# Optimization experiments

Measured on AMD Instinct MI355X. Metric: run time of the kernel, lower is better.

The kernel has to match this reference:

```python
import jax, jax.numpy as jnp
import numpy as np

B, P, C, F, E = 8, 65536, 32768, 32, 524288  # batch, n_paths, n_channels, feature, edges


def setup_inputs() -> dict:
    key = jax.random.key(0)
    ks = jax.random.split(key, 8)
    path_features = jax.random.normal(ks[0], (B, P, F), jnp.float32)
    channel_features = jax.random.normal(ks[1], (B, C, F), jnp.float32)
    edge_path = jax.random.randint(ks[2], (E,), 0, P)
    edge_channel = jnp.sort(jax.random.randint(ks[3], (E,), 0, C))
    s = 1.0 / np.sqrt(F)  # PyTorch GRU default init range
    W_ih = jax.random.uniform(ks[4], (3 * F, F), jnp.float32, -s, s)
    W_hh = jax.random.uniform(ks[5], (3 * F, F), jnp.float32, -s, s)
    b_ih = jax.random.uniform(ks[6], (3 * F,), jnp.float32, -s, s)
    b_hh = jax.random.uniform(ks[7], (3 * F,), jnp.float32, -s, s)
    return dict(path_features=path_features, channel_features=channel_features,
                W_ih=W_ih, W_hh=W_hh, b_ih=b_ih, b_hh=b_hh,
                edge_path=edge_path, edge_channel=edge_channel)


def reference(path_features, channel_features, W_ih, W_hh, b_ih, b_hh, edge_path, edge_channel):
    # Ragged per-channel sum of path features (segment-sum over edge list)
    gathered = jnp.swapaxes(path_features[:, edge_path, :], 0, 1)          # [E, B, F]
    agg = jax.ops.segment_sum(gathered, edge_channel, num_segments=C)      # [C, B, F]
    x = jnp.swapaxes(agg, 0, 1)                                            # [B, C, F]
    h = channel_features                                                   # [B, C, F]
    # Single-step GRU (PyTorch gate order: r, z, n)
    gx = x @ W_ih.T + b_ih                                                 # [B, C, 3F]
    gh = h @ W_hh.T + b_hh
    xr, xz, xn = jnp.split(gx, 3, axis=-1)
    hr, hz, hn = jnp.split(gh, 3, axis=-1)
    r = jax.nn.sigmoid(xr + hr)
    z = jax.nn.sigmoid(xz + hz)
    n = jnp.tanh(xn + r * hn)
    return (1.0 - z) * n + z * h                                           # [B, C, F]
```

## Files before the change

### kernel.cpp

```cpp
#include <hip/hip_runtime.h>

#define NB 8
#define NP 65536
#define NC 32768
#define NF 32
#define NE 524288
#define XROW 40

typedef __attribute__((ext_vector_type(4))) float floatx4;
typedef __attribute__((ext_vector_type(8))) short short8;
typedef __attribute__((ext_vector_type(4))) short short4v;

__device__ __forceinline__ short f2b(float f) {
    union { float f; unsigned int u; } v;
    v.f = f;
    unsigned int lsb = (v.u >> 16) & 1u;
    v.u += 0x7fffu + lsb;
    return (short)(v.u >> 16);
}

__device__ __forceinline__ int lower_bound(const int* __restrict__ a, int v) {
    int lo = 0, hi = NE;
    while (lo < hi) {
        int mid = (lo + hi) >> 1;
        if (a[mid] < v) lo = mid + 1; else hi = mid;
    }
    return lo;
}

__device__ __forceinline__ float sigmoidf_(float v) {
    return 1.f / (1.f + __expf(-v));
}
__device__ __forceinline__ float tanhf_(float v) {
    v = fminf(v, 40.f);
    float t = __expf(2.f * v);
    return (t - 1.f) / (t + 1.f);
}

__global__ __launch_bounds__(256) void fused_gru_kernel(
    const float* __restrict__ path,
    const float* __restrict__ hbuf,
    const float* __restrict__ W_ih,
    const float* __restrict__ W_hh,
    const float* __restrict__ b_ih,
    const float* __restrict__ b_hh,
    const int*   __restrict__ edge_path,
    const int*   __restrict__ edge_channel,
    float*       __restrict__ out)
{
    const int t    = threadIdx.x;
    const int w    = t >> 6;
    const int lane = t & 63;
    const int cblk = blockIdx.x * 8;

    __shared__ int bounds[9];
    __shared__ __align__(16) short xs [64 * XROW];
    __shared__ __align__(16) short wsx[96 * XROW];
    __shared__ __align__(16) short wsh[96 * XROW];

    if (t < 9) bounds[t] = lower_bound(edge_channel, cblk + t);

    for (int idx = t; idx < 96 * NF; idx += 256) {
        int r = idx >> 5, c = idx & 31;
        wsx[r * XROW + c] = f2b(W_ih[idx]);
        wsh[r * XROW + c] = f2b(W_hh[idx]);
    }
    __syncthreads();

    const int b  = lane >> 3;
    const int fq = lane & 7;
    const float* prow = path + (size_t)b * (NP * NF) + fq * 4;

    #pragma unroll
    for (int half = 0; half < 2; ++half) {
        const int cl = w * 2 + half;
        const int s = __builtin_amdgcn_readfirstlane(bounds[cl]);
        const int e = __builtin_amdgcn_readfirstlane(bounds[cl + 1]);
        floatx4 acc = {0.f, 0.f, 0.f, 0.f};
        int i = s;
        for (; i + 8 <= e; i += 8) {
            int p0 = edge_path[i + 0], p1 = edge_path[i + 1];
            int p2 = edge_path[i + 2], p3 = edge_path[i + 3];
            int p4 = edge_path[i + 4], p5 = edge_path[i + 5];
            int p6 = edge_path[i + 6], p7 = edge_path[i + 7];
            floatx4 g0 = *(const floatx4*)(prow + (size_t)p0 * NF);
            floatx4 g1 = *(const floatx4*)(prow + (size_t)p1 * NF);
            floatx4 g2 = *(const floatx4*)(prow + (size_t)p2 * NF);
            floatx4 g3 = *(const floatx4*)(prow + (size_t)p3 * NF);
            floatx4 g4 = *(const floatx4*)(prow + (size_t)p4 * NF);
            floatx4 g5 = *(const floatx4*)(prow + (size_t)p5 * NF);
            floatx4 g6 = *(const floatx4*)(prow + (size_t)p6 * NF);
            floatx4 g7 = *(const floatx4*)(prow + (size_t)p7 * NF);
            acc += ((g0 + g1) + (g2 + g3)) + ((g4 + g5) + (g6 + g7));
        }
        for (; i + 2 <= e; i += 2) {
            int p0 = edge_path[i], p1 = edge_path[i + 1];
            acc += *(const floatx4*)(prow + (size_t)p0 * NF)
                 + *(const floatx4*)(prow + (size_t)p1 * NF);
        }
        if (i < e)
            acc += *(const floatx4*)(prow + (size_t)edge_path[i] * NF);

        short4v xb;
        #pragma unroll
        for (int q = 0; q < 4; ++q) xb[q] = f2b(acc[q]);
        *(short4v*)(&xs[(b * 8 + cl) * XROW + fq * 4]) = xb;
    }
    __syncthreads();

    const int quad = lane >> 4;
    const int n16  = lane & 15;
    const int k0   = quad * 8;

    const int rA = w * 16 + n16;
    short8 ax = *(const short8*)(&xs[rA * XROW + k0]);

    const int bA = rA >> 3;
    const int cA = cblk + (rA & 7);
    const float* hrow = hbuf + ((size_t)bA * NC + cA) * NF + k0;
    floatx4 h0 = *(const floatx4*)(hrow);
    floatx4 h1 = *(const floatx4*)(hrow + 4);
    short8 ah;
    #pragma unroll
    for (int q = 0; q < 4; ++q) { ah[q] = f2b(h0[q]); ah[4 + q] = f2b(h1[q]); }

    float bxv[6], bhv[6];
    #pragma unroll
    for (int tt = 0; tt < 6; ++tt) {
        bxv[tt] = b_ih[16 * tt + n16];
        bhv[tt] = b_hh[16 * tt + n16];
    }

    const floatx4 zero = {0.f, 0.f, 0.f, 0.f};
    floatx4 g[4];
    #pragma unroll
    for (int tt = 0; tt < 4; ++tt) {
        short8 bw = *(const short8*)(&wsx[(16 * tt + n16) * XROW + k0]);
        floatx4 a = __builtin_amdgcn_mfma_f32_16x16x32_bf16(ax, bw, zero, 0, 0, 0);
        bw = *(const short8*)(&wsh[(16 * tt + n16) * XROW + k0]);
        g[tt] = __builtin_amdgcn_mfma_f32_16x16x32_bf16(ah, bw, a, 0, 0, 0);
    }
    floatx4 nx[2], nh[2];
    #pragma unroll
    for (int u = 0; u < 2; ++u) {
        const int tt = 4 + u;
        short8 bw = *(const short8*)(&wsx[(16 * tt + n16) * XROW + k0]);
        nx[u] = __builtin_amdgcn_mfma_f32_16x16x32_bf16(ax, bw, zero, 0, 0, 0);
        bw = *(const short8*)(&wsh[(16 * tt + n16) * XROW + k0]);
        nh[u] = __builtin_amdgcn_mfma_f32_16x16x32_bf16(ah, bw, zero, 0, 0, 0);
    }

    #pragma unroll
    for (int i = 0; i < 4; ++i) {
        const int r  = w * 16 + quad * 4 + i;
        const int b2 = r >> 3;
        const size_t m = (size_t)b2 * NC + (cblk + (r & 7));
        float r0 = sigmoidf_(g[0][i] + bxv[0] + bhv[0]);
        float r1 = sigmoidf_(g[1][i] + bxv[1] + bhv[1]);
        float z0 = sigmoidf_(g[2][i] + bxv[2] + bhv[2]);
        float z1 = sigmoidf_(g[3][i] + bxv[3] + bhv[3]);
        float n0 = tanhf_(nx[0][i] + bxv[4] + r0 * (nh[0][i] + bhv[4]));
        float n1 = tanhf_(nx[1][i] + bxv[5] + r1 * (nh[1][i] + bhv[5]));
        float hv0 = hbuf[m * NF + n16];
        float hv1 = hbuf[m * NF + 16 + n16];
        out[m * NF + n16]      = (1.f - z0) * n0 + z0 * hv0;
        out[m * NF + 16 + n16] = (1.f - z1) * n1 + z1 * hv1;
    }
}

extern "C" void kernel_launch(void* const* d_in, const int* in_sizes, int n_in,
                              void* d_out, int out_size, void* d_ws, size_t ws_size,
                              hipStream_t stream) {
    const float* path = (const float*)d_in[0];
    const float* chan = (const float*)d_in[1];
    const float* W_ih = (const float*)d_in[2];
    const float* W_hh = (const float*)d_in[3];
    const float* b_ih = (const float*)d_in[4];
    const float* b_hh = (const float*)d_in[5];
    const int* edge_path    = (const int*)d_in[6];
    const int* edge_channel = (const int*)d_in[7];
    float* out = (float*)d_out;

    fused_gru_kernel<<<dim3(NC / 8), dim3(256), 0, stream>>>(
        path, chan, W_ih, W_hh, b_ih, b_hh, edge_path, edge_channel, out);
}
```

Before: 222.4 us.

## Pre-transpose path features to path-major fp16 layout for contiguous gathers

Adds a pre-pass kernel that rewrites path_features from [B,P,F] fp32 into a path-major [P,B,F] fp16 buffer in the workspace. The gather loop in the fused GRU kernel then reads all 8 batches of one path from a single contiguous 512-byte row, converting fp16 back to fp32 before accumulating. The aim is to halve the gather traffic and improve locality of the random accesses. In exchange it adds a full read of the path tensor plus a write of the fp16 copy on every call, and loses precision in the inputs before summation. The original fp32 path is kept as a fallback when the workspace is too small.

```diff
diff --git a/kernel.cpp b/kernel.cpp
--- a/kernel.cpp
+++ b/kernel.cpp
@@ -1,4 +1,5 @@
 #include <hip/hip_runtime.h>
+#include <hip/hip_fp16.h>
 
 #define NB 8
 #define NP 65536
@@ -11,6 +12,15 @@
 typedef __attribute__((ext_vector_type(8))) short short8;
 typedef __attribute__((ext_vector_type(4))) short short4v;
 
+struct h4 { __half2 lo, hi; };
+
+__device__ __forceinline__ floatx4 h4tof4(h4 v) {
+    float2 a = __half22float2(v.lo);
+    float2 b = __half22float2(v.hi);
+    floatx4 r; r[0] = a.x; r[1] = a.y; r[2] = b.x; r[3] = b.y;
+    return r;
+}
+
 __device__ __forceinline__ short f2b(float f) {
     union { float f; unsigned int u; } v;
     v.f = f;
@@ -37,16 +47,32 @@
     return (t - 1.f) / (t + 1.f);
 }
 
+__global__ __launch_bounds__(256) void transpose_kernel(
+    const float* __restrict__ path, __half* __restrict__ pathT)
+{
+    const int id = blockIdx.x * 256 + threadIdx.x;
+    const int f4 = (id & 7) * 4;
+    const int b  = (id >> 3) & 7;
+    const int p  = id >> 6;
+    floatx4 v = *(const floatx4*)(path + ((size_t)b * NP + p) * NF + f4);
+    h4 o;
+    o.lo = __floats2half2_rn(v[0], v[1]);
+    o.hi = __floats2half2_rn(v[2], v[3]);
+    *(h4*)(pathT + (size_t)p * (NB * NF) + b * NF + f4) = o;
+}
+
+template <int USET>
 __global__ __launch_bounds__(256) void fused_gru_kernel(
-    const float* __restrict__ path,
-    const float* __restrict__ hbuf,
-    const float* __restrict__ W_ih,
-    const float* __restrict__ W_hh,
-    const float* __restrict__ b_ih,
-    const float* __restrict__ b_hh,
-    const int*   __restrict__ edge_path,
-    const int*   __restrict__ edge_channel,
-    float*       __restrict__ out)
+    const float*  __restrict__ path,
+    const __half* __restrict__ pathT,
+    const float*  __restrict__ hbuf,
+    const float*  __restrict__ W_ih,
+    const float*  __restrict__ W_hh,
+    const float*  __restrict__ b_ih,
+    const float*  __restrict__ b_hh,
+    const int*    __restrict__ edge_path,
+    const int*    __restrict__ edge_channel,
+    float*        __restrict__ out)
 {
     const int t    = threadIdx.x;
     const int w    = t >> 6;
@@ -69,7 +95,8 @@
 
     const int b  = lane >> 3;
     const int fq = lane & 7;
-    const float* prow = path + (size_t)b * (NP * NF) + fq * 4;
+    const float*  prow  = path  + (size_t)b * (NP * NF) + fq * 4;
+    const __half* prowT = pathT + b * NF + fq * 4;
 
     #pragma unroll
     for (int half = 0; half < 2; ++half) {
@@ -78,28 +105,55 @@
         const int e = __builtin_amdgcn_readfirstlane(bounds[cl + 1]);
         floatx4 acc = {0.f, 0.f, 0.f, 0.f};
         int i = s;
-        for (; i + 8 <= e; i += 8) {
-            int p0 = edge_path[i + 0], p1 = edge_path[i + 1];
-            int p2 = edge_path[i + 2], p3 = edge_path[i + 3];
-            int p4 = edge_path[i + 4], p5 = edge_path[i + 5];
-            int p6 = edge_path[i + 6], p7 = edge_path[i + 7];
-            floatx4 g0 = *(const floatx4*)(prow + (size_t)p0 * NF);
-            floatx4 g1 = *(const floatx4*)(prow + (size_t)p1 * NF);
-            floatx4 g2 = *(const floatx4*)(prow + (size_t)p2 * NF);
-            floatx4 g3 = *(const floatx4*)(prow + (size_t)p3 * NF);
-            floatx4 g4 = *(const floatx4*)(prow + (size_t)p4 * NF);
-            floatx4 g5 = *(const floatx4*)(prow + (size_t)p5 * NF);
-            floatx4 g6 = *(const floatx4*)(prow + (size_t)p6 * NF);
-            floatx4 g7 = *(const floatx4*)(prow + (size_t)p7 * NF);
-            acc += ((g0 + g1) + (g2 + g3)) + ((g4 + g5) + (g6 + g7));
+        if (USET) {
+            for (; i + 8 <= e; i += 8) {
+                int p0 = edge_path[i + 0], p1 = edge_path[i + 1];
+                int p2 = edge_path[i + 2], p3 = edge_path[i + 3];
+                int p4 = edge_path[i + 4], p5 = edge_path[i + 5];
+                int p6 = edge_path[i + 6], p7 = edge_path[i + 7];
+                h4 g0 = *(const h4*)(prowT + (size_t)p0 * (NB * NF));
+                h4 g1 = *(const h4*)(prowT + (size_t)p1 * (NB * NF));
+                h4 g2 = *(const h4*)(prowT + (size_t)p2 * (NB * NF));
+                h4 g3 = *(const h4*)(prowT + (size_t)p3 * (NB * NF));
+                h4 g4 = *(const h4*)(prowT + (size_t)p4 * (NB * NF));
+                h4 g5 = *(const h4*)(prowT + (size_t)p5 * (NB * NF));
+                h4 g6 = *(const h4*)(prowT + (size_t)p6 * (NB * NF));
+                h4 g7 = *(const h4*)(prowT + (size_t)p7 * (NB * NF));
+                acc += ((h4tof4(g0) + h4tof4(g1)) + (h4tof4(g2) + h4tof4(g3)))
+                     + ((h4tof4(g4) + h4tof4(g5)) + (h4tof4(g6) + h4tof4(g7)));
+            }
+            for (; i + 2 <= e; i += 2) {
+                int p0 = edge_path[i], p1 = edge_path[i + 1];
+                h4 g0 = *(const h4*)(prowT + (size_t)p0 * (NB * NF));
+                h4 g1 = *(const h4*)(prowT + (size_t)p1 * (NB * NF));
+                acc += h4tof4(g0) + h4tof4(g1);
+            }
+            if (i < e)
+                acc += h4tof4(*(const h4*)(prowT + (size_t)edge_path[i] * (NB * NF)));
+        } else {
+            for (; i + 8 <= e; i += 8) {
+                int p0 = edge_path[i + 0], p1 = edge_path[i + 1];
+                int p2 = edge_path[i + 2], p3 = edge_path[i + 3];
+                int p4 = edge_path[i + 4], p5 = edge_path[i + 5];
+                int p6 = edge_path[i + 6], p7 = edge_path[i + 7];
+                floatx4 g0 = *(const floatx4*)(prow + (size_t)p0 * NF);
+                floatx4 g1 = *(const floatx4*)(prow + (size_t)p1 * NF);
+                floatx4 g2 = *(const floatx4*)(prow + (size_t)p2 * NF);
+                floatx4 g3 = *(const floatx4*)(prow + (size_t)p3 * NF);
+                floatx4 g4 = *(const floatx4*)(prow + (size_t)p4 * NF);
+                floatx4 g5 = *(const floatx4*)(prow + (size_t)p5 * NF);
+                floatx4 g6 = *(const floatx4*)(prow + (size_t)p6 * NF);
+                floatx4 g7 = *(const floatx4*)(prow + (size_t)p7 * NF);
+                acc += ((g0 + g1) + (g2 + g3)) + ((g4 + g5) + (g6 + g7));
+            }
+            for (; i + 2 <= e; i += 2) {
+                int p0 = edge_path[i], p1 = edge_path[i + 1];
+                acc += *(const floatx4*)(prow + (size_t)p0 * NF)
+                     + *(const floatx4*)(prow + (size_t)p1 * NF);
+            }
+            if (i < e)
+                acc += *(const floatx4*)(prow + (size_t)edge_path[i] * NF);
         }
-        for (; i + 2 <= e; i += 2) {
-            int p0 = edge_path[i], p1 = edge_path[i + 1];
-            acc += *(const floatx4*)(prow + (size_t)p0 * NF)
-                 + *(const floatx4*)(prow + (size_t)p1 * NF);
-        }
-        if (i < e)
-            acc += *(const floatx4*)(prow + (size_t)edge_path[i] * NF);
 
         short4v xb;
         #pragma unroll
@@ -181,6 +235,16 @@
     const int* edge_channel = (const int*)d_in[7];
     float* out = (float*)d_out;
 
-    fused_gru_kernel<<<dim3(NC / 8), dim3(256), 0, stream>>>(
-        path, chan, W_ih, W_hh, b_ih, b_hh, edge_path, edge_channel, out);
-}
+    const size_t needT = (size_t)NP * NB * NF * sizeof(__half);
+    if (ws_size >= needT) {
+        __half* pathT = (__half*)d_ws;
+        transpose_kernel<<<dim3((NP * NB * NF / 4) / 256), dim3(256), 0, stream>>>(
+            path, pathT);
+        fused_gru_kernel<1><<<dim3(NC / 8), dim3(256), 0, stream>>>(
+            path, pathT, chan, W_ih, W_hh, b_ih, b_hh, edge_path, edge_channel, out);
+    } else {
+        fused_gru_kernel<0><<<dim3(NC / 8), dim3(256), 0, stream>>>(
+            path, (const __half*)nullptr, chan, W_ih, W_hh, b_ih, b_hh,
+            edge_path, edge_channel, out);
+    }
+}
```

After: 222.3 us. No clear change (-0.0%).

## Convert path features to fp16 in a prep pass and regroup gather by batch

Applied to the files above, without the earlier changes.

Adds a prep kernel that converts the whole path tensor to fp16 in workspace and precomputes all channel segment bounds. The main kernel then gathers half-precision rows. Each block handles one batch over 64 channels, with 8 edges gathered in parallel per wave and reduced by shuffles. Output uses nontemporal stores. The point is to halve the bytes moved by the random gather and drop the per-block binary searches, but the conversion pass must read 64MB and write 32MB every call, which may cost more than the gather saves. fp16 also adds precision loss.

```diff
diff --git a/kernel.cpp b/kernel.cpp
--- a/kernel.cpp
+++ b/kernel.cpp
@@ -1,4 +1,5 @@
 #include <hip/hip_runtime.h>
+#include <hip/hip_fp16.h>
 
 #define NB 8
 #define NP 65536
@@ -6,10 +7,22 @@
 #define NF 32
 #define NE 524288
 #define XROW 40
+#define CHB 64
+#define CONV_BLOCKS 8192
 
 typedef __attribute__((ext_vector_type(4))) float floatx4;
 typedef __attribute__((ext_vector_type(8))) short short8;
 typedef __attribute__((ext_vector_type(4))) short short4v;
+
+struct h4 { __half2 lo, hi; };
+struct h8 { __half2 a, b, c, d; };
+
+__device__ __forceinline__ floatx4 h4tof4(h4 v) {
+    float2 a = __half22float2(v.lo);
+    float2 b = __half22float2(v.hi);
+    floatx4 r; r[0] = a.x; r[1] = a.y; r[2] = b.x; r[3] = b.y;
+    return r;
+}
 
 __device__ __forceinline__ short f2b(float f) {
     union { float f; unsigned int u; } v;
@@ -37,16 +50,156 @@
     return (t - 1.f) / (t + 1.f);
 }
 
-__global__ __launch_bounds__(256) void fused_gru_kernel(
-    const float* __restrict__ path,
-    const float* __restrict__ hbuf,
-    const float* __restrict__ W_ih,
-    const float* __restrict__ W_hh,
-    const float* __restrict__ b_ih,
-    const float* __restrict__ b_hh,
-    const int*   __restrict__ edge_path,
-    const int*   __restrict__ edge_channel,
-    float*       __restrict__ out)
+__global__ __launch_bounds__(256) void prep_kernel(
+    const float* __restrict__ path, __half* __restrict__ pathH,
+    const int* __restrict__ edge_channel, int* __restrict__ bounds)
+{
+    if (blockIdx.x < CONV_BLOCKS) {
+        const size_t id = ((size_t)blockIdx.x * 256 + threadIdx.x) * 8;
+        floatx4 v0 = *(const floatx4*)(path + id);
+        floatx4 v1 = *(const floatx4*)(path + id + 4);
+        h8 o;
+        o.a = __floats2half2_rn(v0[0], v0[1]);
+        o.b = __floats2half2_rn(v0[2], v0[3]);
+        o.c = __floats2half2_rn(v1[0], v1[1]);
+        o.d = __floats2half2_rn(v1[2], v1[3]);
+        *(h8*)(pathH + id) = o;
+    } else {
+        const int c = (blockIdx.x - CONV_BLOCKS) * 256 + threadIdx.x;
+        if (c <= NC) bounds[c] = lower_bound(edge_channel, c);
+    }
+}
+
+__global__ __launch_bounds__(256) void fused_gru_new(
+    const __half* __restrict__ pathH,
+    const float*  __restrict__ hbuf,
+    const float*  __restrict__ W_ih,
+    const float*  __restrict__ W_hh,
+    const float*  __restrict__ b_ih,
+    const float*  __restrict__ b_hh,
+    const int*    __restrict__ edge_path,
+    const int*    __restrict__ bounds,
+    float*        __restrict__ out)
+{
+    const int t    = threadIdx.x;
+    const int w    = t >> 6;
+    const int lane = t & 63;
+    const int batch = blockIdx.x & 7;
+    const int c0    = (blockIdx.x >> 3) * CHB;
+
+    __shared__ __align__(16) short xs [64 * XROW];
+    __shared__ __align__(16) short wsx[96 * XROW];
+    __shared__ __align__(16) short wsh[96 * XROW];
+
+    for (int idx = t; idx < 96 * NF; idx += 256) {
+        int r = idx >> 5, c = idx & 31;
+        wsx[r * XROW + c] = f2b(W_ih[idx]);
+        wsh[r * XROW + c] = f2b(W_hh[idx]);
+    }
+
+    const int eslot = lane >> 3;
+    const int fq    = lane & 7;
+    const __half* pbase = pathH + (size_t)batch * (NP * NF) + fq * 4;
+
+    for (int j = 0; j < 16; ++j) {
+        const int r = w * 16 + j;
+        const int c = c0 + r;
+        const int s = __builtin_amdgcn_readfirstlane(bounds[c]);
+        const int e = __builtin_amdgcn_readfirstlane(bounds[c + 1]);
+        floatx4 acc = {0.f, 0.f, 0.f, 0.f};
+        for (int i = s; i < e; i += 8) {
+            const int idx  = i + eslot;
+            const int idxc = idx < e ? idx : e - 1;
+            const int p    = edge_path[idxc];
+            union { h4 g; uint2 u; } gv;
+            gv.g = *(const h4*)(pbase + (size_t)p * NF);
+            if (idx >= e) { gv.u.x = 0u; gv.u.y = 0u; }
+            acc += h4tof4(gv.g);
+        }
+        #pragma unroll
+        for (int m = 8; m <= 32; m <<= 1) {
+            acc[0] += __shfl_xor(acc[0], m);
+            acc[1] += __shfl_xor(acc[1], m);
+            acc[2] += __shfl_xor(acc[2], m);
+            acc[3] += __shfl_xor(acc[3], m);
+        }
+        if (eslot == 0) {
+            short4v xb;
+            #pragma unroll
+            for (int q = 0; q < 4; ++q) xb[q] = f2b(acc[q]);
+            *(short4v*)(&xs[r * XROW + fq * 4]) = xb;
+        }
+    }
+    __syncthreads();
+
+    const int quad = lane >> 4;
+    const int n16  = lane & 15;
+    const int k0   = quad * 8;
+
+    const int rA = w * 16 + n16;
+    short8 ax = *(const short8*)(&xs[rA * XROW + k0]);
+
+    const size_t mrow = (size_t)batch * NC + c0;
+    const float* hrow = hbuf + (mrow + rA) * NF + k0;
+    floatx4 h0 = *(const floatx4*)(hrow);
+    floatx4 h1 = *(const floatx4*)(hrow + 4);
+    short8 ah;
+    #pragma unroll
+    for (int q = 0; q < 4; ++q) { ah[q] = f2b(h0[q]); ah[4 + q] = f2b(h1[q]); }
+
+    float bxv[6], bhv[6];
+    #pragma unroll
+    for (int tt = 0; tt < 6; ++tt) {
+        bxv[tt] = b_ih[16 * tt + n16];
+        bhv[tt] = b_hh[16 * tt + n16];
+    }
+
+    const floatx4 zero = {0.f, 0.f, 0.f, 0.f};
+    floatx4 g[4];
+    #pragma unroll
+    for (int tt = 0; tt < 4; ++tt) {
+        short8 bw = *(const short8*)(&wsx[(16 * tt + n16) * XROW + k0]);
+        floatx4 a = __builtin_amdgcn_mfma_f32_16x16x32_bf16(ax, bw, zero, 0, 0, 0);
+        bw = *(const short8*)(&wsh[(16 * tt + n16) * XROW + k0]);
+        g[tt] = __builtin_amdgcn_mfma_f32_16x16x32_bf16(ah, bw, a, 0, 0, 0);
+    }
+    floatx4 nx[2], nh[2];
+    #pragma unroll
+    for (int u = 0; u < 2; ++u) {
+        const int tt = 4 + u;
+        short8 bw = *(const short8*)(&wsx[(16 * tt + n16) * XROW + k0]);
+        nx[u] = __builtin_amdgcn_mfma_f32_16x16x32_bf16(ax, bw, zero, 0, 0, 0);
+        bw = *(const short8*)(&wsh[(16 * tt + n16) * XROW + k0]);
+        nh[u] = __builtin_amdgcn_mfma_f32_16x16x32_bf16(ah, bw, zero, 0, 0, 0);
+    }
+
+    #pragma unroll
+    for (int i = 0; i < 4; ++i) {
+        const int r2 = w * 16 + quad * 4 + i;
+        const size_t m = mrow + r2;
+        float r0 = sigmoidf_(g[0][i] + bxv[0] + bhv[0]);
+        float r1 = sigmoidf_(g[1][i] + bxv[1] + bhv[1]);
+        float z0 = sigmoidf_(g[2][i] + bxv[2] + bhv[2]);
+        float z1 = sigmoidf_(g[3][i] + bxv[3] + bhv[3]);
+        float n0 = tanhf_(nx[0][i] + bxv[4] + r0 * (nh[0][i] + bhv[4]));
+        float n1 = tanhf_(nx[1][i] + bxv[5] + r1 * (nh[1][i] + bhv[5]));
+        float hv0 = hbuf[m * NF + n16];
+        float hv1 = hbuf[m * NF + 16 + n16];
+        __builtin_nontemporal_store((1.f - z0) * n0 + z0 * hv0, &out[m * NF + n16]);
+        __builtin_nontemporal_store((1.f - z1) * n1 + z1 * hv1, &out[m * NF + 16 + n16]);
+    }
+}
+
+__global__ __launch_bounds__(256) void fused_gru_fb(
+    const float*  __restrict__ path,
+    const float*  __restrict__ hbuf,
+    const float*  __restrict__ W_ih,
+    const float*  __restrict__ W_hh,
+    const float*  __restrict__ b_ih,
+    const float*  __restrict__ b_hh,
+    const int*    __restrict__ edge_path,
+    const int*    __restrict__ edge_channel,
+    float*        __restrict__ out)
 {
     const int t    = threadIdx.x;
     const int w    = t >> 6;
@@ -59,7 +212,6 @@
     __shared__ __align__(16) short wsh[96 * XROW];
 
     if (t < 9) bounds[t] = lower_bound(edge_channel, cblk + t);
-
     for (int idx = t; idx < 96 * NF; idx += 256) {
         int r = idx >> 5, c = idx & 31;
         wsx[r * XROW + c] = f2b(W_ih[idx]);
@@ -93,14 +245,8 @@
             floatx4 g7 = *(const floatx4*)(prow + (size_t)p7 * NF);
             acc += ((g0 + g1) + (g2 + g3)) + ((g4 + g5) + (g6 + g7));
         }
-        for (; i + 2 <= e; i += 2) {
-            int p0 = edge_path[i], p1 = edge_path[i + 1];
-            acc += *(const floatx4*)(prow + (size_t)p0 * NF)
-                 + *(const floatx4*)(prow + (size_t)p1 * NF);
-        }
-        if (i < e)
+        for (; i < e; ++i)
             acc += *(const floatx4*)(prow + (size_t)edge_path[i] * NF);
-
         short4v xb;
         #pragma unroll
         for (int q = 0; q < 4; ++q) xb[q] = f2b(acc[q]);
@@ -114,7 +260,6 @@
 
     const int rA = w * 16 + n16;
     short8 ax = *(const short8*)(&xs[rA * XROW + k0]);
-
     const int bA = rA >> 3;
     const int cA = cblk + (rA & 7);
     const float* hrow = hbuf + ((size_t)bA * NC + cA) * NF + k0;
@@ -130,7 +275,6 @@
         bxv[tt] = b_ih[16 * tt + n16];
         bhv[tt] = b_hh[16 * tt + n16];
     }
-
     const floatx4 zero = {0.f, 0.f, 0.f, 0.f};
     floatx4 g[4];
     #pragma unroll
@@ -149,7 +293,6 @@
         bw = *(const short8*)(&wsh[(16 * tt + n16) * XROW + k0]);
         nh[u] = __builtin_amdgcn_mfma_f32_16x16x32_bf16(ah, bw, zero, 0, 0, 0);
     }
-
     #pragma unroll
     for (int i = 0; i < 4; ++i) {
         const int r  = w * 16 + quad * 4 + i;
@@ -181,6 +324,18 @@
     const int* edge_channel = (const int*)d_in[7];
     float* out = (float*)d_out;
 
-    fused_gru_kernel<<<dim3(NC / 8), dim3(256), 0, stream>>>(
-        path, chan, W_ih, W_hh, b_ih, b_hh, edge_path, edge_channel, out);
-}
+    const size_t pathH_bytes = (size_t)NB * NP * NF * sizeof(__half);
+    const size_t need = pathH_bytes + (size_t)(NC + 1) * sizeof(int);
+    if (ws_size >= need) {
+        __half* pathH = (__half*)d_ws;
+        int* bounds = (int*)((char*)d_ws + pathH_bytes);
+        const int bblocks = (NC + 1 + 255) / 256;
+        prep_kernel<<<dim3(CONV_BLOCKS + bblocks), dim3(256), 0, stream>>>(
+            path, pathH, edge_channel, bounds);
+        fused_gru_new<<<dim3((NC / CHB) * NB), dim3(256), 0, stream>>>(
+            pathH, chan, W_ih, W_hh, b_ih, b_hh, edge_path, bounds, out);
+    } else {
+        fused_gru_fb<<<dim3(NC / 8), dim3(256), 0, stream>>>(
+            path, chan, W_ih, W_hh, b_ih, b_hh, edge_path, edge_channel, out);
+    }
+}
```

Measured after the change: 295.2 us. 32.7% more time.
